# Performance work log

Hardware: AMD Instinct MI355X
Metric: run time of the kernel (lower is better)

Reference implementation:

```python
import jax, jax.numpy as jnp
import numpy as np


def setup_inputs() -> dict:
    key = jax.random.key(0)
    ks = jax.random.split(key, 13)
    B, W, C = 16, 2048, 512
    inp = {
        "X_sfr": jax.random.normal(ks[0], (B, W, C), dtype=jnp.float32),
        "adj_matrix": jax.random.normal(ks[1], (B, C, C), dtype=jnp.float32),
        "log_temp": jnp.zeros((1,), dtype=jnp.float32),
        "wq": jax.random.normal(ks[2], (1,), dtype=jnp.float32),
        "bq": jax.random.normal(ks[3], (1,), dtype=jnp.float32),
        "wk": jax.random.normal(ks[4], (1,), dtype=jnp.float32),
        "bk": jax.random.normal(ks[5], (1,), dtype=jnp.float32),
        "wv": jax.random.normal(ks[6], (1,), dtype=jnp.float32),
        "bv": jax.random.normal(ks[7], (1,), dtype=jnp.float32),
        "wmu": jax.random.normal(ks[8], (1,), dtype=jnp.float32),
        "bmu": jax.random.normal(ks[9], (1,), dtype=jnp.float32),
        "wsig": jax.random.normal(ks[10], (1,), dtype=jnp.float32),
        "bsig": jax.random.normal(ks[11], (1,), dtype=jnp.float32),
        "k1": 20,
        "k2": 30,
    }
    return inp


def reference(X_sfr, adj_matrix, log_temp, wq, bq, wk, bk, wv, bv, wmu, bmu, wsig, bsig, k1, k2):
    B, W, C = X_sfr.shape
    # spatial propagation: relu + in-degree normalize adjacency
    adj_nonneg = jnp.maximum(adj_matrix, 0.0)
    in_deg = jnp.clip(adj_nonneg.sum(axis=1, keepdims=True), 1e-4)  # [B,1,C]
    adj_norm = adj_nonneg / in_deg
    X_spatial = jnp.einsum('bwi,bij->bwj', X_sfr, adj_norm)  # [B,W,C]

    # static band mask over time: k1 <= |dt| <= k2, fallback to identity rows
    t = jnp.arange(W)
    delta = jnp.abs(t[None, :] - t[:, None])
    band = (delta >= k1) & (delta <= k2)  # [W,W]
    has_valid = band.any(axis=1)
    band = jnp.where(has_valid[:, None], band, jnp.eye(W, dtype=bool))

    # scalar (1->1) q/k/v projections on the temporal token
    temporal_token = X_spatial.mean(axis=2, keepdims=True)  # [B,W,1]
    q = wq * temporal_token + bq                            # [B,W,1]
    k = wk * temporal_token + bk                            # [B,W,1]
    v = wv * X_spatial + bv                                 # [B,W,C]

    temp = jax.nn.softplus(log_temp)[0] + 1e-4
    logits = jnp.matmul(q, jnp.swapaxes(k, 1, 2)) / temp    # [B,W,W] rank-1
    logits = jnp.where(band[None, :, :], logits, -1e9)
    attn = jax.nn.softmax(logits, axis=-1)
    attn = attn * band[None, :, :].astype(attn.dtype)
    attn = attn / (attn.sum(axis=-1, keepdims=True) + 1e-6)

    sacon_scalar = attn.sum(axis=-1, keepdims=True)         # [B,W,1]
    sacon = jnp.broadcast_to(sacon_scalar, (B, W, C))

    X_temporal = jnp.matmul(attn, v)                        # [B,W,C]
    X_fused = X_temporal + X_spatial

    mu = jnp.clip(wmu * X_fused + bmu, -20.0, 20.0)
    sigma_sq = jax.nn.softplus(wsig * X_fused + bsig) + 0.1
    return mu, sigma_sq, sacon
```

## Files before the change

kernel.cpp:

```cpp
#include <hip/hip_runtime.h>
#include <math.h>

#define B_ 16
#define W_ 2048
#define C_ 512

#define OFF_XB    0
#define OFF_BT    33554432
#define OFF_XSP   41943040
#define OFF_INDEG 75497472
#define OFF_TT    75530240

typedef short v8s __attribute__((ext_vector_type(8)));
typedef float v4f __attribute__((ext_vector_type(4)));
typedef unsigned int u32;

__device__ __forceinline__ float softplusf(float x) {
    return fmaxf(x, 0.f) + log1pf(expf(-fabsf(x)));
}
__device__ __forceinline__ unsigned short f2bf(float x) {
    unsigned int u = __float_as_uint(x);
    unsigned int r = (u + 0x7FFFu + ((u >> 16) & 1u)) >> 16;
    return (unsigned short)r;
}
__device__ __forceinline__ float bf2f(unsigned int h) {
    return __uint_as_float(h << 16);
}
__device__ __forceinline__ void gload16(const ushort* g, ushort* l) {
    __builtin_amdgcn_global_load_lds(
        (const __attribute__((address_space(1))) u32*)(g),
        (__attribute__((address_space(3))) u32*)(l), 16, 0, 0);
}

__global__ void indeg_kernel(const float* __restrict__ adj, float* __restrict__ indeg) {
    int b = blockIdx.x;
    int j = blockIdx.y * 256 + threadIdx.x;
    int i0 = blockIdx.z * 64;
    const float* base = adj + (size_t)b * C_ * C_ + (size_t)i0 * C_ + j;
    float s = 0.f;
#pragma unroll 8
    for (int i = 0; i < 64; i++) s += fmaxf(base[(size_t)i * C_], 0.f);
    atomicAdd(&indeg[b * C_ + j], s);
}

__global__ void convertA(const float* __restrict__ X, ushort* __restrict__ Xb) {
    int idx = blockIdx.x * 256 + threadIdx.x;
    float4 v = ((const float4*)X)[idx];
    ushort4 o;
    o.x = f2bf(v.x); o.y = f2bf(v.y); o.z = f2bf(v.z); o.w = f2bf(v.w);
    ((ushort4*)Xb)[idx] = o;
}

__global__ void convertB(const float* __restrict__ adj, const float* __restrict__ indeg,
                         ushort* __restrict__ Bt) {
    __shared__ float t[32][33];
    int b = blockIdx.z, i0 = blockIdx.x * 32, j0 = blockIdx.y * 32;
    int tx = threadIdx.x & 31;
    int ty = threadIdx.x >> 5;
    const float* src = adj + (size_t)b * C_ * C_;
#pragma unroll
    for (int rr = 0; rr < 4; rr++) {
        int ii = ty + rr * 8;
        t[ii][tx] = fmaxf(src[(size_t)(i0 + ii) * C_ + j0 + tx], 0.f);
    }
    __syncthreads();
    int jr0 = threadIdx.x >> 4;
    int ic  = (threadIdx.x & 15) * 2;
#pragma unroll
    for (int pp = 0; pp < 2; pp++) {
        int jr = jr0 + pp * 16;
        float inv = 1.f / fmaxf(indeg[b * C_ + j0 + jr], 1e-4f);
        ushort2 o;
        o.x = f2bf(t[ic][jr] * inv);
        o.y = f2bf(t[ic + 1][jr] * inv);
        *(ushort2*)&Bt[(size_t)b * C_ * C_ + (size_t)(j0 + jr) * C_ + i0 + ic] = o;
    }
}

__global__ __launch_bounds__(256) void gemm_mfma(const ushort* __restrict__ Xb,
                                                 const ushort* __restrict__ Bt,
                                                 ushort* __restrict__ Xsp,
                                                 float* __restrict__ tt) {
    __shared__ ushort As[128 * 32];
    __shared__ ushort Bs[128 * 32];
    const int b  = blockIdx.z;
    const int m0 = blockIdx.y * 128;
    const int n0 = blockIdx.x * 128;
    const int tid  = threadIdx.x;
    const int wave = tid >> 6, lane = tid & 63;
    const int quad = lane >> 4, l16 = lane & 15;
    const int mw = (wave & 1) * 64, nw = (wave >> 1) * 64;

    const ushort* Ag = Xb + (size_t)b * W_ * C_ + (size_t)m0 * C_;
    const ushort* Bg = Bt + (size_t)b * C_ * C_ + (size_t)n0 * C_;

    const int sm = tid >> 2;
    const int sk = (tid & 3) * 8;

    v4f acc[4][4];
#pragma unroll
    for (int mt = 0; mt < 4; mt++)
#pragma unroll
        for (int nt = 0; nt < 4; nt++)
            acc[mt][nt] = (v4f){0.f, 0.f, 0.f, 0.f};

    for (int k0 = 0; k0 < C_; k0 += 32) {
        __syncthreads();
        gload16(Ag + (size_t)sm * C_ + k0 + sk,        As + tid * 8);
        gload16(Ag + (size_t)(sm + 64) * C_ + k0 + sk, As + 2048 + tid * 8);
        gload16(Bg + (size_t)sm * C_ + k0 + sk,        Bs + tid * 8);
        gload16(Bg + (size_t)(sm + 64) * C_ + k0 + sk, Bs + 2048 + tid * 8);
        __syncthreads();

        v8s af[4], bf[4];
#pragma unroll
        for (int mt = 0; mt < 4; mt++)
            af[mt] = *(const v8s*)&As[(mw + mt * 16 + l16) * 32 + quad * 8];
#pragma unroll
        for (int nt = 0; nt < 4; nt++)
            bf[nt] = *(const v8s*)&Bs[(nw + nt * 16 + l16) * 32 + quad * 8];
#pragma unroll
        for (int mt = 0; mt < 4; mt++)
#pragma unroll
            for (int nt = 0; nt < 4; nt++)
                acc[mt][nt] = __builtin_amdgcn_mfma_f32_16x16x32_bf16(af[mt], bf[nt], acc[mt][nt], 0, 0, 0);
    }

#pragma unroll
    for (int mt = 0; mt < 4; mt++) {
#pragma unroll
        for (int nt = 0; nt < 4; nt++) {
            int col = n0 + nw + nt * 16 + l16;
#pragma unroll
            for (int r = 0; r < 4; r++) {
                int row = m0 + mw + mt * 16 + quad * 4 + r;
                Xsp[((size_t)b * W_ + row) * C_ + col] = f2bf(acc[mt][nt][r]);
            }
        }
    }

#pragma unroll
    for (int mt = 0; mt < 4; mt++) {
#pragma unroll
        for (int r = 0; r < 4; r++) {
            float s = acc[mt][0][r] + acc[mt][1][r] + acc[mt][2][r] + acc[mt][3][r];
            s += __shfl_xor(s, 1);
            s += __shfl_xor(s, 2);
            s += __shfl_xor(s, 4);
            s += __shfl_xor(s, 8);
            if (l16 == 0) {
                int row = m0 + mw + mt * 16 + quad * 4 + r;
                atomicAdd(&tt[b * W_ + row], s);
            }
        }
    }
}

__global__ __launch_bounds__(256) void final_kernel(const ushort* __restrict__ Xsp,
                                                    const float* __restrict__ tt,
                                                    const float* __restrict__ ltp,
                                                    const float* __restrict__ wqp, const float* __restrict__ bqp,
                                                    const float* __restrict__ wkp, const float* __restrict__ bkp,
                                                    const float* __restrict__ wvp, const float* __restrict__ bvp,
                                                    const float* __restrict__ wmup, const float* __restrict__ bmup,
                                                    const float* __restrict__ wsigp, const float* __restrict__ bsigp,
                                                    const int* __restrict__ k1p, const int* __restrict__ k2p,
                                                    float* __restrict__ out) {
    __shared__ float wsh[4][32];
    __shared__ float Ssh[4];
    const int wid = threadIdx.x >> 6, lane = threadIdx.x & 63;
    const int row = blockIdx.x * 4 + wid;
    const int b = row >> 11, i = row & (W_ - 1);
    const int K1 = k1p[0], K2 = k2p[0];
    int ns = K2 - K1 + 1;
    if (ns > 16) ns = 16;
    const int n2 = 2 * ns;

    if (lane < 32) {
        const float cinv = 1.f / C_;
        const float temp = softplusf(ltp[0]) + 1e-4f;
        const float invt = 1.f / temp;
        const float q = (wqp[0] * cinv) * tt[row] + bqp[0];
        const float wk = wkp[0] * cinv, bk = bkp[0];
        const float* ttb = tt + b * W_;
        int s = lane;
        int j = (s < ns) ? (i - K2 + s) : (i + K1 + (s - ns));
        bool valid = (s < n2) && (j >= 0) && (j < W_);
        float l = valid ? (q * (wk * ttb[j] + bk) * invt) : -INFINITY;
        float mx = l;
#pragma unroll
        for (int off = 16; off > 0; off >>= 1) mx = fmaxf(mx, __shfl_xor(mx, off, 32));
        float e = valid ? expf(l - mx) : 0.f;
        float T = e;
#pragma unroll
        for (int off = 16; off > 0; off >>= 1) T += __shfl_xor(T, off, 32);
        float p = e / T;
        float S = p;
#pragma unroll
        for (int off = 16; off > 0; off >>= 1) S += __shfl_xor(S, off, 32);
        float rn = 1.f / (S + 1e-6f);
        wsh[wid][lane] = p * rn;
        if (lane == 0) Ssh[wid] = S * rn;
    }
    __syncthreads();

    const ushort* Xbp = Xsp + (size_t)b * W_ * C_;
    const int c8 = lane * 8;
    float a[8] = {0.f, 0.f, 0.f, 0.f, 0.f, 0.f, 0.f, 0.f};
    for (int s = 0; s < n2; s++) {
        float w = wsh[wid][s];
        int j = (s < ns) ? (i - K2 + s) : (i + K1 + (s - ns));
        j = min(max(j, 0), W_ - 1);
        uint4 v = *(const uint4*)(Xbp + (size_t)j * C_ + c8);
        a[0] = fmaf(w, bf2f(v.x & 0xffff), a[0]);
        a[1] = fmaf(w, bf2f(v.x >> 16),    a[1]);
        a[2] = fmaf(w, bf2f(v.y & 0xffff), a[2]);
        a[3] = fmaf(w, bf2f(v.y >> 16),    a[3]);
        a[4] = fmaf(w, bf2f(v.z & 0xffff), a[4]);
        a[5] = fmaf(w, bf2f(v.z >> 16),    a[5]);
        a[6] = fmaf(w, bf2f(v.w & 0xffff), a[6]);
        a[7] = fmaf(w, bf2f(v.w >> 16),    a[7]);
    }
    const float S = Ssh[wid];
    const float wv = wvp[0], bv = bvp[0];
    const float wmu = wmup[0], bmu = bmup[0];
    const float wsig = wsigp[0], bsig = bsigp[0];

    uint4 xv = *(const uint4*)(Xbp + (size_t)i * C_ + c8);
    float xs[8];
    xs[0] = bf2f(xv.x & 0xffff); xs[1] = bf2f(xv.x >> 16);
    xs[2] = bf2f(xv.y & 0xffff); xs[3] = bf2f(xv.y >> 16);
    xs[4] = bf2f(xv.z & 0xffff); xs[5] = bf2f(xv.z >> 16);
    xs[6] = bf2f(xv.w & 0xffff); xs[7] = bf2f(xv.w >> 16);

    float mu[8], sg[8];
#pragma unroll
    for (int k = 0; k < 8; k++) {
        float xf = fmaf(wv, a[k], bv * S) + xs[k];
        mu[k] = fminf(fmaxf(fmaf(wmu, xf, bmu), -20.f), 20.f);
        sg[k] = softplusf(fmaf(wsig, xf, bsig)) + 0.1f;
    }

    const size_t N = (size_t)B_ * W_ * C_;
    const size_t base = (size_t)row * C_ + c8;
    *(float4*)&out[base]     = (float4){mu[0], mu[1], mu[2], mu[3]};
    *(float4*)&out[base + 4] = (float4){mu[4], mu[5], mu[6], mu[7]};
    *(float4*)&out[N + base]     = (float4){sg[0], sg[1], sg[2], sg[3]};
    *(float4*)&out[N + base + 4] = (float4){sg[4], sg[5], sg[6], sg[7]};
    *(float4*)&out[2 * N + base]     = (float4){S, S, S, S};
    *(float4*)&out[2 * N + base + 4] = (float4){S, S, S, S};
}

extern "C" void kernel_launch(void* const* d_in, const int* in_sizes, int n_in,
                              void* d_out, int out_size, void* d_ws, size_t ws_size,
                              hipStream_t stream) {
    const float* X_sfr = (const float*)d_in[0];
    const float* adj   = (const float*)d_in[1];
    const float* ltp   = (const float*)d_in[2];
    const float* wq    = (const float*)d_in[3];
    const float* bq    = (const float*)d_in[4];
    const float* wk    = (const float*)d_in[5];
    const float* bk    = (const float*)d_in[6];
    const float* wv    = (const float*)d_in[7];
    const float* bv    = (const float*)d_in[8];
    const float* wmu   = (const float*)d_in[9];
    const float* bmu   = (const float*)d_in[10];
    const float* wsig  = (const float*)d_in[11];
    const float* bsig  = (const float*)d_in[12];
    const int*   k1p   = (const int*)d_in[13];
    const int*   k2p   = (const int*)d_in[14];

    char* ws = (char*)d_ws;
    ushort* Xb    = (ushort*)(ws + OFF_XB);
    ushort* Bt    = (ushort*)(ws + OFF_BT);
    ushort* Xsp   = (ushort*)(ws + OFF_XSP);
    float*  indeg = (float*)(ws + OFF_INDEG);
    float*  tt    = (float*)(ws + OFF_TT);
    float*  out   = (float*)d_out;

    hipMemsetAsync(indeg, 0, (B_ * C_ + B_ * W_) * sizeof(float), stream);

    indeg_kernel<<<dim3(B_, C_ / 256, 8), 256, 0, stream>>>(adj, indeg);

    convertA<<<(B_ * W_ * C_ / 4) / 256, 256, 0, stream>>>(X_sfr, Xb);

    convertB<<<dim3(C_ / 32, C_ / 32, B_), 256, 0, stream>>>(adj, indeg, Bt);

    gemm_mfma<<<dim3(C_ / 128, W_ / 128, B_), 256, 0, stream>>>(Xb, Bt, Xsp, tt);

    final_kernel<<<(B_ * W_) / 4, 256, 0, stream>>>(Xsp, tt, ltp, wq, bq, wk, bk,
                                                    wv, bv, wmu, bmu, wsig, bsig,
                                                    k1p, k2p, out);
}
```

Baseline: 391.1 us.

## Fuse adjacency degree and conversion kernels; compute four rows per wave in final kernel

The in-degree reduction and the normalize/transpose/bf16 conversion of the adjacency are merged into one kernel, with one block per 32-column strip per batch. This removes the atomics, one launch and the indeg buffer. The final kernel now has each wave produce four consecutive output rows, so each loaded band row of X_spatial is shared across them through a widened weight table in LDS with zero padding. This cuts redundant global loads in the band gather. The cost is more registers for the accumulators and only 256 blocks for the adjacency prep, which may underfill the GPU.

```diff
diff --git a/kernel.cpp b/kernel.cpp
--- a/kernel.cpp
+++ b/kernel.cpp
@@ -8,8 +8,7 @@
 #define OFF_XB    0
 #define OFF_BT    33554432
 #define OFF_XSP   41943040
-#define OFF_INDEG 75497472
-#define OFF_TT    75530240
+#define OFF_TT    75497472
 
 typedef short v8s __attribute__((ext_vector_type(8)));
 typedef float v4f __attribute__((ext_vector_type(4)));
@@ -32,15 +31,47 @@
         (__attribute__((address_space(3))) u32*)(l), 16, 0, 0);
 }
 
-__global__ void indeg_kernel(const float* __restrict__ adj, float* __restrict__ indeg) {
-    int b = blockIdx.x;
-    int j = blockIdx.y * 256 + threadIdx.x;
-    int i0 = blockIdx.z * 64;
-    const float* base = adj + (size_t)b * C_ * C_ + (size_t)i0 * C_ + j;
+__global__ __launch_bounds__(256) void prep_adj(const float* __restrict__ adj,
+                                                ushort* __restrict__ Bt) {
+    __shared__ float cs[8][32];
+    __shared__ float inv[32];
+    __shared__ float t[32][33];
+    const int b = blockIdx.y, j0 = blockIdx.x * 32;
+    const int tx = threadIdx.x & 31, ty = threadIdx.x >> 5;
+    const float* src = adj + (size_t)b * C_ * C_;
+
     float s = 0.f;
-#pragma unroll 8
-    for (int i = 0; i < 64; i++) s += fmaxf(base[(size_t)i * C_], 0.f);
-    atomicAdd(&indeg[b * C_ + j], s);
+#pragma unroll 4
+    for (int it = 0; it < C_ / 8; it++)
+        s += fmaxf(src[(size_t)(it * 8 + ty) * C_ + j0 + tx], 0.f);
+    cs[ty][tx] = s;
+    __syncthreads();
+    if (ty == 0) {
+        float tot = cs[0][tx] + cs[1][tx] + cs[2][tx] + cs[3][tx]
+                  + cs[4][tx] + cs[5][tx] + cs[6][tx] + cs[7][tx];
+        inv[tx] = 1.f / fmaxf(tot, 1e-4f);
+    }
+
+    const int jr = threadIdx.x >> 4;
+    const int ic = (threadIdx.x & 15) * 2;
+    for (int i0t = 0; i0t < C_; i0t += 32) {
+        __syncthreads();
+#pragma unroll
+        for (int rr = 0; rr < 4; rr++) {
+            int ii = ty + rr * 8;
+            t[ii][tx] = fmaxf(src[(size_t)(i0t + ii) * C_ + j0 + tx], 0.f);
+        }
+        __syncthreads();
+#pragma unroll
+        for (int pp = 0; pp < 2; pp++) {
+            int j = jr + pp * 16;
+            float iv = inv[j];
+            ushort2 o;
+            o.x = f2bf(t[ic][j] * iv);
+            o.y = f2bf(t[ic + 1][j] * iv);
+            *(ushort2*)&Bt[(size_t)b * C_ * C_ + (size_t)(j0 + j) * C_ + i0t + ic] = o;
+        }
+    }
 }
 
 __global__ void convertA(const float* __restrict__ X, ushort* __restrict__ Xb) {
@@ -49,32 +80,6 @@
     ushort4 o;
     o.x = f2bf(v.x); o.y = f2bf(v.y); o.z = f2bf(v.z); o.w = f2bf(v.w);
     ((ushort4*)Xb)[idx] = o;
-}
-
-__global__ void convertB(const float* __restrict__ adj, const float* __restrict__ indeg,
-                         ushort* __restrict__ Bt) {
-    __shared__ float t[32][33];
-    int b = blockIdx.z, i0 = blockIdx.x * 32, j0 = blockIdx.y * 32;
-    int tx = threadIdx.x & 31;
-    int ty = threadIdx.x >> 5;
-    const float* src = adj + (size_t)b * C_ * C_;
-#pragma unroll
-    for (int rr = 0; rr < 4; rr++) {
-        int ii = ty + rr * 8;
-        t[ii][tx] = fmaxf(src[(size_t)(i0 + ii) * C_ + j0 + tx], 0.f);
-    }
-    __syncthreads();
-    int jr0 = threadIdx.x >> 4;
-    int ic  = (threadIdx.x & 15) * 2;
-#pragma unroll
-    for (int pp = 0; pp < 2; pp++) {
-        int jr = jr0 + pp * 16;
-        float inv = 1.f / fmaxf(indeg[b * C_ + j0 + jr], 1e-4f);
-        ushort2 o;
-        o.x = f2bf(t[ic][jr] * inv);
-        o.y = f2bf(t[ic + 1][jr] * inv);
-        *(ushort2*)&Bt[(size_t)b * C_ * C_ + (size_t)(j0 + jr) * C_ + i0 + ic] = o;
-    }
 }
 
 __global__ __launch_bounds__(256) void gemm_mfma(const ushort* __restrict__ Xb,
@@ -166,89 +171,112 @@
                                                     const float* __restrict__ wsigp, const float* __restrict__ bsigp,
                                                     const int* __restrict__ k1p, const int* __restrict__ k2p,
                                                     float* __restrict__ out) {
-    __shared__ float wsh[4][32];
-    __shared__ float Ssh[4];
+    __shared__ float wlds[4][4][40];
+    __shared__ float Ssh[4][4];
     const int wid = threadIdx.x >> 6, lane = threadIdx.x & 63;
-    const int row = blockIdx.x * 4 + wid;
-    const int b = row >> 11, i = row & (W_ - 1);
+    const int i0w = blockIdx.x * 16 + wid * 4;
+    const int b = i0w >> 11, ib = i0w & (W_ - 1);
     const int K1 = k1p[0], K2 = k2p[0];
     int ns = K2 - K1 + 1;
     if (ns > 16) ns = 16;
     const int n2 = 2 * ns;
+    const int nsL = ns + 3;
+    const int nu = 2 * nsL;
+
+    for (int k = threadIdx.x; k < 4 * 4 * 40; k += 256) ((float*)wlds)[k] = 0.f;
+    __syncthreads();
 
     if (lane < 32) {
         const float cinv = 1.f / C_;
         const float temp = softplusf(ltp[0]) + 1e-4f;
         const float invt = 1.f / temp;
-        const float q = (wqp[0] * cinv) * tt[row] + bqp[0];
-        const float wk = wkp[0] * cinv, bk = bkp[0];
+        const float wkc = wkp[0] * cinv, bk = bkp[0];
+        const float wqc = wqp[0] * cinv, bq = bqp[0];
         const float* ttb = tt + b * W_;
-        int s = lane;
-        int j = (s < ns) ? (i - K2 + s) : (i + K1 + (s - ns));
-        bool valid = (s < n2) && (j >= 0) && (j < W_);
-        float l = valid ? (q * (wk * ttb[j] + bk) * invt) : -INFINITY;
-        float mx = l;
-#pragma unroll
-        for (int off = 16; off > 0; off >>= 1) mx = fmaxf(mx, __shfl_xor(mx, off, 32));
-        float e = valid ? expf(l - mx) : 0.f;
-        float T = e;
-#pragma unroll
-        for (int off = 16; off > 0; off >>= 1) T += __shfl_xor(T, off, 32);
-        float p = e / T;
-        float S = p;
-#pragma unroll
-        for (int off = 16; off > 0; off >>= 1) S += __shfl_xor(S, off, 32);
-        float rn = 1.f / (S + 1e-6f);
-        wsh[wid][lane] = p * rn;
-        if (lane == 0) Ssh[wid] = S * rn;
+        for (int r = 0; r < 4; r++) {
+            const int i = ib + r;
+            const float q = wqc * ttb[i] + bq;
+            int s = lane;
+            int j = (s < ns) ? (i - K2 + s) : (i + K1 + (s - ns));
+            bool valid = (s < n2) && (j >= 0) && (j < W_);
+            float l = valid ? (q * (wkc * ttb[j] + bk) * invt) : -INFINITY;
+            float mx = l;
+#pragma unroll
+            for (int off = 16; off > 0; off >>= 1) mx = fmaxf(mx, __shfl_xor(mx, off, 32));
+            float e = valid ? expf(l - mx) : 0.f;
+            float T = e;
+#pragma unroll
+            for (int off = 16; off > 0; off >>= 1) T += __shfl_xor(T, off, 32);
+            float p = e / T;
+            float S = p;
+#pragma unroll
+            for (int off = 16; off > 0; off >>= 1) S += __shfl_xor(S, off, 32);
+            float rn = 1.f / (S + 1e-6f);
+            if (s < n2) {
+                int u = (s < ns) ? (r + s) : (nsL + r + (s - ns));
+                wlds[wid][r][u] = p * rn;
+            }
+            if (lane == 0) Ssh[wid][r] = S * rn;
+        }
     }
     __syncthreads();
 
     const ushort* Xbp = Xsp + (size_t)b * W_ * C_;
     const int c8 = lane * 8;
-    float a[8] = {0.f, 0.f, 0.f, 0.f, 0.f, 0.f, 0.f, 0.f};
-    for (int s = 0; s < n2; s++) {
-        float w = wsh[wid][s];
-        int j = (s < ns) ? (i - K2 + s) : (i + K1 + (s - ns));
+    float acc[4][8];
+#pragma unroll
+    for (int r = 0; r < 4; r++)
+#pragma unroll
+        for (int k = 0; k < 8; k++) acc[r][k] = 0.f;
+
+    for (int u = 0; u < nu; u++) {
+        int j = (u < nsL) ? (ib - K2 + u) : (ib + K1 + (u - nsL));
         j = min(max(j, 0), W_ - 1);
         uint4 v = *(const uint4*)(Xbp + (size_t)j * C_ + c8);
-        a[0] = fmaf(w, bf2f(v.x & 0xffff), a[0]);
-        a[1] = fmaf(w, bf2f(v.x >> 16),    a[1]);
-        a[2] = fmaf(w, bf2f(v.y & 0xffff), a[2]);
-        a[3] = fmaf(w, bf2f(v.y >> 16),    a[3]);
-        a[4] = fmaf(w, bf2f(v.z & 0xffff), a[4]);
-        a[5] = fmaf(w, bf2f(v.z >> 16),    a[5]);
-        a[6] = fmaf(w, bf2f(v.w & 0xffff), a[6]);
-        a[7] = fmaf(w, bf2f(v.w >> 16),    a[7]);
-    }
-    const float S = Ssh[wid];
+        float x[8];
+        x[0] = bf2f(v.x & 0xffff); x[1] = bf2f(v.x >> 16);
+        x[2] = bf2f(v.y & 0xffff); x[3] = bf2f(v.y >> 16);
+        x[4] = bf2f(v.z & 0xffff); x[5] = bf2f(v.z >> 16);
+        x[6] = bf2f(v.w & 0xffff); x[7] = bf2f(v.w >> 16);
+#pragma unroll
+        for (int r = 0; r < 4; r++) {
+            float w = wlds[wid][r][u];
+#pragma unroll
+            for (int k = 0; k < 8; k++) acc[r][k] = fmaf(w, x[k], acc[r][k]);
+        }
+    }
+
     const float wv = wvp[0], bv = bvp[0];
     const float wmu = wmup[0], bmu = bmup[0];
     const float wsig = wsigp[0], bsig = bsigp[0];
-
-    uint4 xv = *(const uint4*)(Xbp + (size_t)i * C_ + c8);
-    float xs[8];
-    xs[0] = bf2f(xv.x & 0xffff); xs[1] = bf2f(xv.x >> 16);
-    xs[2] = bf2f(xv.y & 0xffff); xs[3] = bf2f(xv.y >> 16);
-    xs[4] = bf2f(xv.z & 0xffff); xs[5] = bf2f(xv.z >> 16);
-    xs[6] = bf2f(xv.w & 0xffff); xs[7] = bf2f(xv.w >> 16);
-
-    float mu[8], sg[8];
-#pragma unroll
-    for (int k = 0; k < 8; k++) {
-        float xf = fmaf(wv, a[k], bv * S) + xs[k];
-        mu[k] = fminf(fmaxf(fmaf(wmu, xf, bmu), -20.f), 20.f);
-        sg[k] = softplusf(fmaf(wsig, xf, bsig)) + 0.1f;
-    }
-
     const size_t N = (size_t)B_ * W_ * C_;
-    const size_t base = (size_t)row * C_ + c8;
-    *(float4*)&out[base]     = (float4){mu[0], mu[1], mu[2], mu[3]};
-    *(float4*)&out[base + 4] = (float4){mu[4], mu[5], mu[6], mu[7]};
-    *(float4*)&out[N + base]     = (float4){sg[0], sg[1], sg[2], sg[3]};
-    *(float4*)&out[N + base + 4] = (float4){sg[4], sg[5], sg[6], sg[7]};
-    *(float4*)&out[2 * N + base]     = (float4){S, S, S, S};
-    *(float4*)&out[2 * N + base + 4] = (float4){S, S, S, S};
+
+#pragma unroll
+    for (int r = 0; r < 4; r++) {
+        const float S = Ssh[wid][r];
+        uint4 xv = *(const uint4*)(Xbp + (size_t)(ib + r) * C_ + c8);
+        float xs[8];
+        xs[0] = bf2f(xv.x & 0xffff); xs[1] = bf2f(xv.x >> 16);
+        xs[2] = bf2f(xv.y & 0xffff); xs[3] = bf2f(xv.y >> 16);
+        xs[4] = bf2f(xv.z & 0xffff); xs[5] = bf2f(xv.z >> 16);
+        xs[6] = bf2f(xv.w & 0xffff); xs[7] = bf2f(xv.w >> 16);
+
+        float mu[8], sg[8];
+#pragma unroll
+        for (int k = 0; k < 8; k++) {
+            float xf = fmaf(wv, acc[r][k], bv * S) + xs[k];
+            mu[k] = fminf(fmaxf(fmaf(wmu, xf, bmu), -20.f), 20.f);
+            sg[k] = softplusf(fmaf(wsig, xf, bsig)) + 0.1f;
+        }
+
+        const size_t base = (size_t)(i0w + r) * C_ + c8;
+        *(float4*)&out[base]     = (float4){mu[0], mu[1], mu[2], mu[3]};
+        *(float4*)&out[base + 4] = (float4){mu[4], mu[5], mu[6], mu[7]};
+        *(float4*)&out[N + base]     = (float4){sg[0], sg[1], sg[2], sg[3]};
+        *(float4*)&out[N + base + 4] = (float4){sg[4], sg[5], sg[6], sg[7]};
+        *(float4*)&out[2 * N + base]     = (float4){S, S, S, S};
+        *(float4*)&out[2 * N + base + 4] = (float4){S, S, S, S};
+    }
 }
 
 extern "C" void kernel_launch(void* const* d_in, const int* in_sizes, int n_in,
@@ -271,24 +299,21 @@
     const int*   k2p   = (const int*)d_in[14];
 
     char* ws = (char*)d_ws;
-    ushort* Xb    = (ushort*)(ws + OFF_XB);
-    ushort* Bt    = (ushort*)(ws + OFF_BT);
-    ushort* Xsp   = (ushort*)(ws + OFF_XSP);
-    float*  indeg = (float*)(ws + OFF_INDEG);
-    float*  tt    = (float*)(ws + OFF_TT);
-    float*  out   = (float*)d_out;
-
-    hipMemsetAsync(indeg, 0, (B_ * C_ + B_ * W_) * sizeof(float), stream);
-
-    indeg_kernel<<<dim3(B_, C_ / 256, 8), 256, 0, stream>>>(adj, indeg);
+    ushort* Xb  = (ushort*)(ws + OFF_XB);
+    ushort* Bt  = (ushort*)(ws + OFF_BT);
+    ushort* Xsp = (ushort*)(ws + OFF_XSP);
+    float*  tt  = (float*)(ws + OFF_TT);
+    float*  out = (float*)d_out;
+
+    hipMemsetAsync(tt, 0, B_ * W_ * sizeof(float), stream);
+
+    prep_adj<<<dim3(C_ / 32, B_), 256, 0, stream>>>(adj, Bt);
 
     convertA<<<(B_ * W_ * C_ / 4) / 256, 256, 0, stream>>>(X_sfr, Xb);
 
-    convertB<<<dim3(C_ / 32, C_ / 32, B_), 256, 0, stream>>>(adj, indeg, Bt);
-
     gemm_mfma<<<dim3(C_ / 128, W_ / 128, B_), 256, 0, stream>>>(Xb, Bt, Xsp, tt);
 
-    final_kernel<<<(B_ * W_) / 4, 256, 0, stream>>>(Xsp, tt, ltp, wq, bq, wk, bk,
-                                                    wv, bv, wmu, bmu, wsig, bsig,
-                                                    k1p, k2p, out);
-}
+    final_kernel<<<(B_ * W_) / 16, 256, 0, stream>>>(Xsp, tt, ltp, wq, bq, wk, bk,
+                                                     wv, bv, wmu, bmu, wsig, bsig,
+                                                     k1p, k2p, out);
+}
```

Result: no change. 383.8 us (-1.9%).
